# Kernel tuning notes

Hardware: AMD Instinct MI355X
Metric: run time of the kernel (lower is better)

Reference implementation:

```python
import jax, jax.numpy as jnp
import numpy as np

ALPHA = 5.0  # spatial bandwidth
BETA = 5.0   # feature (bilateral) bandwidth
EPS = 1e-20


def gauss_filter(features, values):
    """Exact dense Gaussian (bilateral) filter: the math the permutohedral
    lattice (pl.apply) approximates.
    features: [B, D, N], values: [B, C, N] -> [B, C, N]
    Q[b,c,i] = sum_j exp(-0.5*||f_i - f_j||^2) * v[b,c,j]
    """
    sq = jnp.sum(features * features, axis=1)  # [B, N]
    d2 = sq[:, :, None] + sq[:, None, :] - 2.0 * jnp.einsum('bdi,bdj->bij', features, features)
    K = jnp.exp(-0.5 * jnp.maximum(d2, 0.0))  # [B, N, N]
    return jnp.einsum('bij,bcj->bci', K, values)


def setup_inputs() -> dict:
    key = jax.random.key(0)
    k1, k2 = jax.random.split(key)
    I = jax.random.normal(k1, (2, 3, 18, 18, 18), dtype=jnp.float32)
    U = jax.random.normal(k2, (2, 4, 18, 18, 18), dtype=jnp.float32)
    return {"I": I, "U": U}


def reference(I, U):
    B, n_feat, X, Y, Z = I.shape
    N = X * Y * Z
    n_ch = U.shape[1]
    # spatial coordinates, scaled by alpha (smoothness kernel part)
    gx, gy, gz = jnp.meshgrid(jnp.arange(X), jnp.arange(Y), jnp.arange(Z), indexing='ij')
    coords = jnp.stack([gx, gy, gz], 0).astype(I.dtype)            # [3, X, Y, Z]
    coords = jnp.broadcast_to(coords[None], (B, 3, X, Y, Z))
    feats = jnp.concatenate([coords / ALPHA, I / BETA], axis=1)    # [B, 3+n_feat, X, Y, Z]
    feats = feats.reshape(B, n_feat + 3, N)
    # normalization: filter an all-ones signal (use_norm=True path)
    ones = jnp.ones((B, 1, N), dtype=I.dtype)
    spatial_norm = 1.0 / jnp.sqrt(gauss_filter(feats, ones) + EPS)  # [B, 1, N]
    # unary -> softmax over channels
    Uf = U.reshape(B, n_ch, N)
    H1 = jax.nn.softmax(Uf, axis=1)                                 # [B, C, N]
    # pairwise message passing (normalized bilateral filter)
    Q1 = gauss_filter(feats, H1 * spatial_norm) * spatial_norm      # [B, C, N]
    # trace(Q1_flat.T @ (1 - H1_flat)) == elementwise sum (same reshape on both)
    loss = jnp.sum(Q1 * (1.0 - H1))
    return loss
```

## Files before the change

### kernel.cpp

```cpp
#include <hip/hip_runtime.h>

#define B_     2
#define NCH    4
#define DIMX   18
#define NPT    (18*18*18)
#define TIL    183
#define ITIL   184
#define NPTP   (ITIL*32)
#define IBLOCKS 46
#define JSP    12
#define FSC    (1.2011224087864498f / 5.0f)
#define QPAD   -30000.0f

typedef __attribute__((ext_vector_type(8)))  short short8;
typedef __attribute__((ext_vector_type(4)))  short short4_;
typedef __attribute__((ext_vector_type(16))) float f32x16;
typedef __attribute__((ext_vector_type(4)))  int   int4_;

#define EXP2(x) __builtin_amdgcn_exp2f(x)
#define MFMA32(a, b, c) __builtin_amdgcn_mfma_f32_32x32x16_bf16(a, b, c, 0, 0, 0)

__device__ __forceinline__ unsigned short bf16rtn(float f) {
  unsigned u = __float_as_uint(f);
  u += 0x7fffu + ((u >> 16) & 1u);
  return (unsigned short)(u >> 16);
}
__device__ __forceinline__ float bf2f(unsigned short s) {
  return __uint_as_float(((unsigned)s) << 16);
}

__device__ __forceinline__ float blockReduceSum(float v) {
  #pragma unroll
  for (int o = 32; o > 0; o >>= 1) v += __shfl_down(v, o, 64);
  __shared__ float red[4];
  int wid = threadIdx.x >> 6, lane = threadIdx.x & 63;
  if (lane == 0) red[wid] = v;
  __syncthreads();
  v = (threadIdx.x < 4) ? red[threadIdx.x] : 0.0f;
  if (wid == 0) {
    v += __shfl_down(v, 2, 64);
    v += __shfl_down(v, 1, 64);
  }
  return v;
}

__global__ void prep_kernel(const float* __restrict__ I, const float* __restrict__ U,
                            short8* __restrict__ AHI, short8* __restrict__ ALO,
                            short8* __restrict__ BHL, float4* __restrict__ H) {
  int idx = blockIdx.x * 256 + threadIdx.x;
  if (idx >= B_ * NPTP) return;
  int bb = idx / NPTP, n = idx - bb * NPTP;
  short8 ahi, alo, bhi, blo;
  float4 hh;
  if (n < NPT) {
    int x = n / (DIMX * DIMX);
    int rem = n - x * DIMX * DIMX;
    int y = rem / DIMX, z = rem - y * DIMX;
    float f0 = x * FSC, f1 = y * FSC, f2 = z * FSC;
    float f3 = I[(size_t)(bb * 3 + 0) * NPT + n] * FSC;
    float f4 = I[(size_t)(bb * 3 + 1) * NPT + n] * FSC;
    float f5 = I[(size_t)(bb * 3 + 2) * NPT + n] * FSC;
    float q = -0.5f * (f0*f0 + f1*f1 + f2*f2 + f3*f3 + f4*f4 + f5*f5);
    float av[8] = {f0, f1, f2, f3, f4, f5, q, 1.0f};
    float bv[8] = {f0, f1, f2, f3, f4, f5, 1.0f, q};
    #pragma unroll
    for (int e = 0; e < 8; ++e) {
      unsigned short ah = bf16rtn(av[e]);
      ahi[e] = (short)ah;
      alo[e] = (short)bf16rtn(av[e] - bf2f(ah));
      unsigned short bh = bf16rtn(bv[e]);
      bhi[e] = (short)bh;
      blo[e] = (short)bf16rtn(bv[e] - bf2f(bh));
    }
    float u0 = U[(size_t)(bb * NCH + 0) * NPT + n];
    float u1 = U[(size_t)(bb * NCH + 1) * NPT + n];
    float u2 = U[(size_t)(bb * NCH + 2) * NPT + n];
    float u3 = U[(size_t)(bb * NCH + 3) * NPT + n];
    float m = fmaxf(fmaxf(u0, u1), fmaxf(u2, u3));
    float e0 = __expf(u0 - m), e1 = __expf(u1 - m), e2 = __expf(u2 - m), e3 = __expf(u3 - m);
    float inv = 1.0f / (e0 + e1 + e2 + e3);
    hh = make_float4(e0 * inv, e1 * inv, e2 * inv, e3 * inv);
  } else {
    #pragma unroll
    for (int e = 0; e < 8; ++e) { ahi[e] = 0; alo[e] = 0; bhi[e] = 0; blo[e] = 0; }
    bhi[7] = (short)bf16rtn(QPAD);
    hh = make_float4(0.f, 0.f, 0.f, 0.f);
  }
  AHI[idx] = ahi;
  ALO[idx] = alo;
  BHL[(size_t)idx * 2]     = bhi;
  BHL[(size_t)idx * 2 + 1] = blo;
  H[idx] = hh;
}

__global__ void __launch_bounds__(256) pass1_kernel(const short8* __restrict__ AHI,
                                                    const short8* __restrict__ ALO,
                                                    const short8* __restrict__ BHL,
                                                    float* __restrict__ part) {
  int tid = threadIdx.x, wid = tid >> 6, l = tid & 63, h = l >> 5, li = l & 31;
  int bb = blockIdx.z, ch = blockIdx.y;
  int it = blockIdx.x * 4 + wid;
  int i = it * 32 + li;
  size_t pbase = (size_t)bb * NPTP;

  short8 zer = {0, 0, 0, 0, 0, 0, 0, 0};
  short8 b1 = AHI[pbase + i];
  short8 b2 = h ? zer : ALO[pbase + i];

  int t0 = ch * TIL / JSP, t1 = (ch + 1) * TIL / JSP;
  float sacc = 0.0f;
  for (int t = t0; t < t1; ++t) {
    int j = t * 32 + li;
    short8 a1 = BHL[(pbase + j) * 2 + h];
    f32x16 acc;
    #pragma unroll
    for (int r = 0; r < 16; ++r) acc[r] = 0.0f;
    acc = MFMA32(a1, b1, acc);
    acc = MFMA32(a1, b2, acc);
    float ssum = 0.0f;
    #pragma unroll
    for (int r = 0; r < 16; ++r) ssum += EXP2(acc[r]);
    sacc += ssum;
  }
  sacc += __shfl_xor(sacc, 32, 64);
  if (h == 0) part[((size_t)bb * JSP + ch) * NPTP + i] = sacc;
}

__global__ void finalize_kernel(const float4* __restrict__ H, const float* __restrict__ part,
                                unsigned short* __restrict__ Vt, float4* __restrict__ G4) {
  int idx = blockIdx.x * 256 + threadIdx.x;
  if (idx >= B_ * NPTP) return;
  int bb = idx / NPTP, i = idx - bb * NPTP;
  if (i < NPT) {
    float s = 0.0f;
    #pragma unroll
    for (int k = 0; k < JSP; ++k) s += part[((size_t)bb * JSP + k) * NPTP + i];
    float nrm = rsqrtf(s + 1e-20f);
    float4 hh = H[idx];
    Vt[((size_t)bb * 4 + 0) * NPTP + i] = bf16rtn(hh.x * nrm);
    Vt[((size_t)bb * 4 + 1) * NPTP + i] = bf16rtn(hh.y * nrm);
    Vt[((size_t)bb * 4 + 2) * NPTP + i] = bf16rtn(hh.z * nrm);
    Vt[((size_t)bb * 4 + 3) * NPTP + i] = bf16rtn(hh.w * nrm);
    G4[idx] = make_float4((1.0f - hh.x) * nrm, (1.0f - hh.y) * nrm,
                          (1.0f - hh.z) * nrm, (1.0f - hh.w) * nrm);
  } else {
    Vt[((size_t)bb * 4 + 0) * NPTP + i] = 0;
    Vt[((size_t)bb * 4 + 1) * NPTP + i] = 0;
    Vt[((size_t)bb * 4 + 2) * NPTP + i] = 0;
    Vt[((size_t)bb * 4 + 3) * NPTP + i] = 0;
    G4[idx] = make_float4(0.f, 0.f, 0.f, 0.f);
  }
}

__global__ void __launch_bounds__(256) pass2_kernel(const short8* __restrict__ AHI,
                                                    const short8* __restrict__ ALO,
                                                    const short8* __restrict__ BHL,
                                                    const unsigned short* __restrict__ Vt,
                                                    const float4* __restrict__ G4,
                                                    float* __restrict__ partialLoss) {
  int tid = threadIdx.x, wid = tid >> 6, l = tid & 63, h = l >> 5, li = l & 31;
  int bb = blockIdx.z, ch = blockIdx.y;
  int it = blockIdx.x * 4 + wid;
  int i = it * 32 + li;
  size_t pbase = (size_t)bb * NPTP;

  short8 zer = {0, 0, 0, 0, 0, 0, 0, 0};
  short4_ zer4 = {0, 0, 0, 0};
  short8 b1 = AHI[pbase + i];
  short8 b2 = h ? zer : ALO[pbase + i];
  float4 g = G4[pbase + i];

  bool cok = li < 4;
  const unsigned short* vrow = Vt + ((size_t)bb * 4 + (cok ? li : 0)) * NPTP;

  f32x16 d2;
  #pragma unroll
  for (int r = 0; r < 16; ++r) d2[r] = 0.0f;

  int t0 = ch * TIL / JSP, t1 = (ch + 1) * TIL / JSP;
  for (int t = t0; t < t1; ++t) {
    int j32 = t * 32;
    short8 a1 = BHL[(pbase + j32 + li) * 2 + h];
    f32x16 acc;
    #pragma unroll
    for (int r = 0; r < 16; ++r) acc[r] = 0.0f;
    acc = MFMA32(a1, b1, acc);
    acc = MFMA32(a1, b2, acc);
    float w[16];
    #pragma unroll
    for (int r = 0; r < 16; ++r) w[r] = EXP2(acc[r]);

    int p[8];
    #pragma unroll
    for (int r = 0; r < 8; ++r)
      asm("v_cvt_pk_bf16_f32 %0, %1, %2" : "=v"(p[r]) : "v"(w[2*r]), "v"(w[2*r+1]));
    union { int4_ iv; short8 sv; } u1, u2;
    u1.iv = (int4_){p[0], p[1], p[2], p[3]};
    u2.iv = (int4_){p[4], p[5], p[6], p[7]};

    short4_ va = cok ? *(const short4_*)(vrow + j32 + 4*h)      : zer4;
    short4_ vb = cok ? *(const short4_*)(vrow + j32 + 8 + 4*h)  : zer4;
    short4_ vc = cok ? *(const short4_*)(vrow + j32 + 16 + 4*h) : zer4;
    short4_ vd = cok ? *(const short4_*)(vrow + j32 + 24 + 4*h) : zer4;
    short8 vf1, vf2;
    #pragma unroll
    for (int e = 0; e < 4; ++e) {
      vf1[e] = va[e]; vf1[4 + e] = vb[e];
      vf2[e] = vc[e]; vf2[4 + e] = vd[e];
    }
    d2 = MFMA32(vf1, u1.sv, d2);
    d2 = MFMA32(vf2, u2.sv, d2);
  }

  float loss = d2[0] * g.x + d2[1] * g.y + d2[2] * g.z + d2[3] * g.w;
  float r = blockReduceSum(loss);
  if (tid == 0)
    partialLoss[((size_t)bb * JSP + ch) * IBLOCKS + blockIdx.x] = r;
}

__global__ void reduce_kernel(const float* __restrict__ partialLoss, int n,
                              float* __restrict__ out) {
  float v = 0.0f;
  for (int k = threadIdx.x; k < n; k += 256) v += partialLoss[k];
  float r = blockReduceSum(v);
  if (threadIdx.x == 0) out[0] = r;
}

extern "C" void kernel_launch(void* const* d_in, const int* in_sizes, int n_in,
                              void* d_out, int out_size, void* d_ws, size_t ws_size,
                              hipStream_t stream) {
  const float* I = (const float*)d_in[0];
  const float* U = (const float*)d_in[1];
  float* out = (float*)d_out;

  char* w = (char*)d_ws;
  short8* AHI = (short8*)w;          w += (size_t)B_ * NPTP * 16;
  short8* ALO = (short8*)w;          w += (size_t)B_ * NPTP * 16;
  short8* BHL = (short8*)w;          w += (size_t)B_ * NPTP * 32;
  float4* H   = (float4*)w;          w += (size_t)B_ * NPTP * 16;
  float*  part = (float*)w;          w += (size_t)B_ * JSP * NPTP * 4;
  unsigned short* Vt = (unsigned short*)w; w += (size_t)B_ * 4 * NPTP * 2;
  float4* G4  = (float4*)w;          w += (size_t)B_ * NPTP * 16;
  float*  pl  = (float*)w;           w += (size_t)B_ * JSP * IBLOCKS * 4;

  prep_kernel<<<(B_ * NPTP + 255) / 256, 256, 0, stream>>>(I, U, AHI, ALO, BHL, H);
  dim3 grid(IBLOCKS, JSP, B_);
  pass1_kernel<<<grid, 256, 0, stream>>>(AHI, ALO, BHL, part);
  finalize_kernel<<<(B_ * NPTP + 255) / 256, 256, 0, stream>>>(H, part, Vt, G4);
  pass2_kernel<<<grid, 256, 0, stream>>>(AHI, ALO, BHL, Vt, G4, pl);
  reduce_kernel<<<1, 256, 0, stream>>>(pl, B_ * JSP * IBLOCKS, out);
}
```

Before: 46.78 us.

## Process two i-tiles per wave and prefetch next j-tile in both passes

Each wave in pass1 and pass2 now computes two 32-row i-tiles against every loaded j-tile. This reuses the BHL and V operand loads and gives the scheduler two independent MFMA/exp chains. The next j-tile's operands are loaded one iteration ahead to hide global-load latency, and the exp sums use a tree reduction. To keep the grid size unchanged, the i-block count is halved and the j-split is doubled. That doubles the partial-sum buffer that finalize must read, and holding two tiles' state raises register pressure.

```diff
diff --git a/kernel.cpp b/kernel.cpp
--- a/kernel.cpp
+++ b/kernel.cpp
@@ -1,16 +1,17 @@
 #include <hip/hip_runtime.h>
 
-#define B_     2
-#define NCH    4
-#define DIMX   18
-#define NPT    (18*18*18)
-#define TIL    183
-#define ITIL   184
-#define NPTP   (ITIL*32)
-#define IBLOCKS 46
-#define JSP    12
-#define FSC    (1.2011224087864498f / 5.0f)
-#define QPAD   -30000.0f
+#define B_      2
+#define NCH     4
+#define DIMX    18
+#define NPT     (18*18*18)
+#define TIL     183
+#define ITIL    184
+#define NPTP    (ITIL*32)
+#define IBLOCKS 23
+#define JSP     24
+#define NB      (IBLOCKS*JSP*B_)
+#define FSC     (1.2011224087864498f / 5.0f)
+#define QPAD    -30000.0f
 
 typedef __attribute__((ext_vector_type(8)))  short short8;
 typedef __attribute__((ext_vector_type(4)))  short short4_;
@@ -47,6 +48,7 @@
 __global__ void prep_kernel(const float* __restrict__ I, const float* __restrict__ U,
                             short8* __restrict__ AHI, short8* __restrict__ ALO,
                             short8* __restrict__ BHL, float4* __restrict__ H) {
+  const short8 zer = {0, 0, 0, 0, 0, 0, 0, 0};
   int idx = blockIdx.x * 256 + threadIdx.x;
   if (idx >= B_ * NPTP) return;
   int bb = idx / NPTP, n = idx - bb * NPTP;
@@ -77,12 +79,11 @@
     float u2 = U[(size_t)(bb * NCH + 2) * NPT + n];
     float u3 = U[(size_t)(bb * NCH + 3) * NPT + n];
     float m = fmaxf(fmaxf(u0, u1), fmaxf(u2, u3));
-    float e0 = __expf(u0 - m), e1 = __expf(u1 - m), e2 = __expf(u2 - m), e3 = __expf(u3 - m);
+    float e0 = __expf(u0-m), e1 = __expf(u1-m), e2 = __expf(u2-m), e3 = __expf(u3-m);
     float inv = 1.0f / (e0 + e1 + e2 + e3);
-    hh = make_float4(e0 * inv, e1 * inv, e2 * inv, e3 * inv);
+    hh = make_float4(e0*inv, e1*inv, e2*inv, e3*inv);
   } else {
-    #pragma unroll
-    for (int e = 0; e < 8; ++e) { ahi[e] = 0; alo[e] = 0; bhi[e] = 0; blo[e] = 0; }
+    ahi = zer; alo = zer; bhi = zer; blo = zer;
     bhi[7] = (short)bf16rtn(QPAD);
     hh = make_float4(0.f, 0.f, 0.f, 0.f);
   }
@@ -93,63 +94,123 @@
   H[idx] = hh;
 }
 
+__device__ __forceinline__ void arg_tile(const short8 a, const short8 b1, const short8 b2,
+                                         f32x16* acc) {
+  f32x16 c;
+  #pragma unroll
+  for (int r = 0; r < 16; ++r) c[r] = 0.0f;
+  c = MFMA32(a, b1, c);
+  c = MFMA32(a, b2, c);
+  *acc = c;
+}
+
+__device__ __forceinline__ float expsum16(const f32x16 acc) {
+  float e[16];
+  #pragma unroll
+  for (int r = 0; r < 16; ++r) e[r] = EXP2(acc[r]);
+  float s8[8];
+  #pragma unroll
+  for (int r = 0; r < 8; ++r) s8[r] = e[2*r] + e[2*r+1];
+  float s4[4];
+  #pragma unroll
+  for (int r = 0; r < 4; ++r) s4[r] = s8[2*r] + s8[2*r+1];
+  return (s4[0] + s4[1]) + (s4[2] + s4[3]);
+}
+
 __global__ void __launch_bounds__(256) pass1_kernel(const short8* __restrict__ AHI,
                                                     const short8* __restrict__ ALO,
                                                     const short8* __restrict__ BHL,
                                                     float* __restrict__ part) {
+  const short8 zer = {0, 0, 0, 0, 0, 0, 0, 0};
   int tid = threadIdx.x, wid = tid >> 6, l = tid & 63, h = l >> 5, li = l & 31;
-  int bb = blockIdx.z, ch = blockIdx.y;
-  int it = blockIdx.x * 4 + wid;
-  int i = it * 32 + li;
+  int bb = blockIdx.z, jc = blockIdx.y;
+  int i0 = (blockIdx.x * 8 + wid) * 32 + li;
+  int i1 = i0 + 128;
   size_t pbase = (size_t)bb * NPTP;
-
-  short8 zer = {0, 0, 0, 0, 0, 0, 0, 0};
-  short8 b1 = AHI[pbase + i];
-  short8 b2 = h ? zer : ALO[pbase + i];
-
-  int t0 = ch * TIL / JSP, t1 = (ch + 1) * TIL / JSP;
-  float sacc = 0.0f;
+  int t0 = jc * TIL / JSP, t1 = (jc + 1) * TIL / JSP;
+
+  short8 b1_0 = AHI[pbase + i0];
+  short8 b2_0 = h ? zer : ALO[pbase + i0];
+  short8 b1_1 = AHI[pbase + i1];
+  short8 b2_1 = h ? zer : ALO[pbase + i1];
+
+  float sacc0 = 0.0f, sacc1 = 0.0f;
+  short8 a_cur = BHL[(pbase + (size_t)t0 * 32 + li) * 2 + h];
   for (int t = t0; t < t1; ++t) {
-    int j = t * 32 + li;
-    short8 a1 = BHL[(pbase + j) * 2 + h];
-    f32x16 acc;
-    #pragma unroll
-    for (int r = 0; r < 16; ++r) acc[r] = 0.0f;
-    acc = MFMA32(a1, b1, acc);
-    acc = MFMA32(a1, b2, acc);
-    float ssum = 0.0f;
-    #pragma unroll
-    for (int r = 0; r < 16; ++r) ssum += EXP2(acc[r]);
-    sacc += ssum;
-  }
-  sacc += __shfl_xor(sacc, 32, 64);
-  if (h == 0) part[((size_t)bb * JSP + ch) * NPTP + i] = sacc;
+    short8 a_nxt = (t + 1 < t1) ? BHL[(pbase + (size_t)(t+1) * 32 + li) * 2 + h] : zer;
+    f32x16 acc0, acc1;
+    arg_tile(a_cur, b1_0, b2_0, &acc0);
+    arg_tile(a_cur, b1_1, b2_1, &acc1);
+    sacc0 += expsum16(acc0);
+    sacc1 += expsum16(acc1);
+    a_cur = a_nxt;
+  }
+  sacc0 += __shfl_xor(sacc0, 32, 64);
+  sacc1 += __shfl_xor(sacc1, 32, 64);
+  if (h == 0) {
+    part[((size_t)bb * JSP + jc) * NPTP + i0] = sacc0;
+    part[((size_t)bb * JSP + jc) * NPTP + i1] = sacc1;
+  }
 }
 
 __global__ void finalize_kernel(const float4* __restrict__ H, const float* __restrict__ part,
                                 unsigned short* __restrict__ Vt, float4* __restrict__ G4) {
   int idx = blockIdx.x * 256 + threadIdx.x;
   if (idx >= B_ * NPTP) return;
-  int bb = idx / NPTP, i = idx - bb * NPTP;
-  if (i < NPT) {
+  int bb = idx / NPTP, ii = idx - bb * NPTP;
+  if (ii < NPT) {
     float s = 0.0f;
     #pragma unroll
-    for (int k = 0; k < JSP; ++k) s += part[((size_t)bb * JSP + k) * NPTP + i];
+    for (int k = 0; k < JSP; ++k) s += part[((size_t)bb * JSP + k) * NPTP + ii];
     float nrm = rsqrtf(s + 1e-20f);
     float4 hh = H[idx];
-    Vt[((size_t)bb * 4 + 0) * NPTP + i] = bf16rtn(hh.x * nrm);
-    Vt[((size_t)bb * 4 + 1) * NPTP + i] = bf16rtn(hh.y * nrm);
-    Vt[((size_t)bb * 4 + 2) * NPTP + i] = bf16rtn(hh.z * nrm);
-    Vt[((size_t)bb * 4 + 3) * NPTP + i] = bf16rtn(hh.w * nrm);
+    Vt[((size_t)bb * 4 + 0) * NPTP + ii] = bf16rtn(hh.x * nrm);
+    Vt[((size_t)bb * 4 + 1) * NPTP + ii] = bf16rtn(hh.y * nrm);
+    Vt[((size_t)bb * 4 + 2) * NPTP + ii] = bf16rtn(hh.z * nrm);
+    Vt[((size_t)bb * 4 + 3) * NPTP + ii] = bf16rtn(hh.w * nrm);
     G4[idx] = make_float4((1.0f - hh.x) * nrm, (1.0f - hh.y) * nrm,
                           (1.0f - hh.z) * nrm, (1.0f - hh.w) * nrm);
   } else {
-    Vt[((size_t)bb * 4 + 0) * NPTP + i] = 0;
-    Vt[((size_t)bb * 4 + 1) * NPTP + i] = 0;
-    Vt[((size_t)bb * 4 + 2) * NPTP + i] = 0;
-    Vt[((size_t)bb * 4 + 3) * NPTP + i] = 0;
+    Vt[((size_t)bb * 4 + 0) * NPTP + ii] = 0;
+    Vt[((size_t)bb * 4 + 1) * NPTP + ii] = 0;
+    Vt[((size_t)bb * 4 + 2) * NPTP + ii] = 0;
+    Vt[((size_t)bb * 4 + 3) * NPTP + ii] = 0;
     G4[idx] = make_float4(0.f, 0.f, 0.f, 0.f);
   }
+}
+
+__device__ __forceinline__ void ldv(const unsigned short* __restrict__ vrow, int j32,
+                                    int h, bool cok, short8* vf1, short8* vf2) {
+  const short4_ zer4 = {0, 0, 0, 0};
+  short4_ va = cok ? *(const short4_*)(vrow + j32 + 4*h)      : zer4;
+  short4_ vb = cok ? *(const short4_*)(vrow + j32 + 8 + 4*h)  : zer4;
+  short4_ vc = cok ? *(const short4_*)(vrow + j32 + 16 + 4*h) : zer4;
+  short4_ vd = cok ? *(const short4_*)(vrow + j32 + 24 + 4*h) : zer4;
+  short8 f1, f2;
+  #pragma unroll
+  for (int e = 0; e < 4; ++e) {
+    f1[e] = va[e]; f1[4 + e] = vb[e];
+    f2[e] = vc[e]; f2[4 + e] = vd[e];
+  }
+  *vf1 = f1; *vf2 = f2;
+}
+
+__device__ __forceinline__ void pv_tile(const f32x16 acc, const short8 vf1,
+                                        const short8 vf2, f32x16* d2) {
+  float w[16];
+  #pragma unroll
+  for (int r = 0; r < 16; ++r) w[r] = EXP2(acc[r]);
+  int p[8];
+  #pragma unroll
+  for (int r = 0; r < 8; ++r)
+    asm("v_cvt_pk_bf16_f32 %0, %1, %2" : "=v"(p[r]) : "v"(w[2*r]), "v"(w[2*r+1]));
+  union { int4_ iv; short8 sv; } u1, u2;
+  u1.iv = (int4_){p[0], p[1], p[2], p[3]};
+  u2.iv = (int4_){p[4], p[5], p[6], p[7]};
+  f32x16 d = *d2;
+  d = MFMA32(vf1, u1.sv, d);
+  d = MFMA32(vf2, u2.sv, d);
+  *d2 = d;
 }
 
 __global__ void __launch_bounds__(256) pass2_kernel(const short8* __restrict__ AHI,
@@ -157,71 +218,55 @@
                                                     const short8* __restrict__ BHL,
                                                     const unsigned short* __restrict__ Vt,
                                                     const float4* __restrict__ G4,
-                                                    float* __restrict__ partialLoss) {
+                                                    float* __restrict__ pl) {
+  const short8 zer = {0, 0, 0, 0, 0, 0, 0, 0};
   int tid = threadIdx.x, wid = tid >> 6, l = tid & 63, h = l >> 5, li = l & 31;
-  int bb = blockIdx.z, ch = blockIdx.y;
-  int it = blockIdx.x * 4 + wid;
-  int i = it * 32 + li;
+  int bb = blockIdx.z, jc = blockIdx.y;
+  int i0 = (blockIdx.x * 8 + wid) * 32 + li;
+  int i1 = i0 + 128;
   size_t pbase = (size_t)bb * NPTP;
-
-  short8 zer = {0, 0, 0, 0, 0, 0, 0, 0};
-  short4_ zer4 = {0, 0, 0, 0};
-  short8 b1 = AHI[pbase + i];
-  short8 b2 = h ? zer : ALO[pbase + i];
-  float4 g = G4[pbase + i];
-
+  int t0 = jc * TIL / JSP, t1 = (jc + 1) * TIL / JSP;
+
+  short8 b1_0 = AHI[pbase + i0];
+  short8 b2_0 = h ? zer : ALO[pbase + i0];
+  short8 b1_1 = AHI[pbase + i1];
+  short8 b2_1 = h ? zer : ALO[pbase + i1];
+  float4 g0 = G4[pbase + i0];
+  float4 g1 = G4[pbase + i1];
   bool cok = li < 4;
   const unsigned short* vrow = Vt + ((size_t)bb * 4 + (cok ? li : 0)) * NPTP;
 
-  f32x16 d2;
-  #pragma unroll
-  for (int r = 0; r < 16; ++r) d2[r] = 0.0f;
-
-  int t0 = ch * TIL / JSP, t1 = (ch + 1) * TIL / JSP;
+  f32x16 d2_0, d2_1;
+  #pragma unroll
+  for (int r = 0; r < 16; ++r) { d2_0[r] = 0.0f; d2_1[r] = 0.0f; }
+
+  short8 a_cur = BHL[(pbase + (size_t)t0 * 32 + li) * 2 + h];
+  short8 vf1c, vf2c;
+  ldv(vrow, t0 * 32, h, cok, &vf1c, &vf2c);
+
   for (int t = t0; t < t1; ++t) {
-    int j32 = t * 32;
-    short8 a1 = BHL[(pbase + j32 + li) * 2 + h];
-    f32x16 acc;
-    #pragma unroll
-    for (int r = 0; r < 16; ++r) acc[r] = 0.0f;
-    acc = MFMA32(a1, b1, acc);
-    acc = MFMA32(a1, b2, acc);
-    float w[16];
-    #pragma unroll
-    for (int r = 0; r < 16; ++r) w[r] = EXP2(acc[r]);
-
-    int p[8];
-    #pragma unroll
-    for (int r = 0; r < 8; ++r)
-      asm("v_cvt_pk_bf16_f32 %0, %1, %2" : "=v"(p[r]) : "v"(w[2*r]), "v"(w[2*r+1]));
-    union { int4_ iv; short8 sv; } u1, u2;
-    u1.iv = (int4_){p[0], p[1], p[2], p[3]};
-    u2.iv = (int4_){p[4], p[5], p[6], p[7]};
-
-    short4_ va = cok ? *(const short4_*)(vrow + j32 + 4*h)      : zer4;
-    short4_ vb = cok ? *(const short4_*)(vrow + j32 + 8 + 4*h)  : zer4;
-    short4_ vc = cok ? *(const short4_*)(vrow + j32 + 16 + 4*h) : zer4;
-    short4_ vd = cok ? *(const short4_*)(vrow + j32 + 24 + 4*h) : zer4;
-    short8 vf1, vf2;
-    #pragma unroll
-    for (int e = 0; e < 4; ++e) {
-      vf1[e] = va[e]; vf1[4 + e] = vb[e];
-      vf2[e] = vc[e]; vf2[4 + e] = vd[e];
+    short8 a_nxt = zer, vf1n = zer, vf2n = zer;
+    if (t + 1 < t1) {
+      a_nxt = BHL[(pbase + (size_t)(t+1) * 32 + li) * 2 + h];
+      ldv(vrow, (t + 1) * 32, h, cok, &vf1n, &vf2n);
     }
-    d2 = MFMA32(vf1, u1.sv, d2);
-    d2 = MFMA32(vf2, u2.sv, d2);
-  }
-
-  float loss = d2[0] * g.x + d2[1] * g.y + d2[2] * g.z + d2[3] * g.w;
+    f32x16 acc0, acc1;
+    arg_tile(a_cur, b1_0, b2_0, &acc0);
+    arg_tile(a_cur, b1_1, b2_1, &acc1);
+    pv_tile(acc0, vf1c, vf2c, &d2_0);
+    pv_tile(acc1, vf1c, vf2c, &d2_1);
+    a_cur = a_nxt; vf1c = vf1n; vf2c = vf2n;
+  }
+
+  float loss = d2_0[0] * g0.x + d2_0[1] * g0.y + d2_0[2] * g0.z + d2_0[3] * g0.w
+             + d2_1[0] * g1.x + d2_1[1] * g1.y + d2_1[2] * g1.z + d2_1[3] * g1.w;
   float r = blockReduceSum(loss);
-  if (tid == 0)
-    partialLoss[((size_t)bb * JSP + ch) * IBLOCKS + blockIdx.x] = r;
-}
-
-__global__ void reduce_kernel(const float* __restrict__ partialLoss, int n,
-                              float* __restrict__ out) {
+  if (tid == 0) pl[((size_t)bb * JSP + jc) * IBLOCKS + blockIdx.x] = r;
+}
+
+__global__ void reduce_kernel(const float* __restrict__ pl, int n, float* __restrict__ out) {
   float v = 0.0f;
-  for (int k = threadIdx.x; k < n; k += 256) v += partialLoss[k];
+  for (int k = threadIdx.x; k < n; k += 256) v += pl[k];
   float r = blockReduceSum(v);
   if (threadIdx.x == 0) out[0] = r;
 }
@@ -234,19 +279,19 @@
   float* out = (float*)d_out;
 
   char* w = (char*)d_ws;
-  short8* AHI = (short8*)w;          w += (size_t)B_ * NPTP * 16;
-  short8* ALO = (short8*)w;          w += (size_t)B_ * NPTP * 16;
-  short8* BHL = (short8*)w;          w += (size_t)B_ * NPTP * 32;
-  float4* H   = (float4*)w;          w += (size_t)B_ * NPTP * 16;
-  float*  part = (float*)w;          w += (size_t)B_ * JSP * NPTP * 4;
-  unsigned short* Vt = (unsigned short*)w; w += (size_t)B_ * 4 * NPTP * 2;
-  float4* G4  = (float4*)w;          w += (size_t)B_ * NPTP * 16;
-  float*  pl  = (float*)w;           w += (size_t)B_ * JSP * IBLOCKS * 4;
+  short8* AHI = (short8*)w;                 w += (size_t)B_ * NPTP * 16;
+  short8* ALO = (short8*)w;                 w += (size_t)B_ * NPTP * 16;
+  short8* BHL = (short8*)w;                 w += (size_t)B_ * NPTP * 32;
+  float4* H   = (float4*)w;                 w += (size_t)B_ * NPTP * 16;
+  float*  part = (float*)w;                 w += (size_t)B_ * JSP * NPTP * 4;
+  unsigned short* Vt = (unsigned short*)w;  w += (size_t)B_ * 4 * NPTP * 2;
+  float4* G4  = (float4*)w;                 w += (size_t)B_ * NPTP * 16;
+  float*  pl  = (float*)w;                  w += (size_t)NB * 4;
 
   prep_kernel<<<(B_ * NPTP + 255) / 256, 256, 0, stream>>>(I, U, AHI, ALO, BHL, H);
   dim3 grid(IBLOCKS, JSP, B_);
   pass1_kernel<<<grid, 256, 0, stream>>>(AHI, ALO, BHL, part);
   finalize_kernel<<<(B_ * NPTP + 255) / 256, 256, 0, stream>>>(H, part, Vt, G4);
   pass2_kernel<<<grid, 256, 0, stream>>>(AHI, ALO, BHL, Vt, G4, pl);
-  reduce_kernel<<<1, 256, 0, stream>>>(pl, B_ * JSP * IBLOCKS, out);
-}
+  reduce_kernel<<<1, 256, 0, stream>>>(pl, NB, out);
+}
```

After: 45.64 us. 2.4% less time.
